# Kernel tuning notes

Measured on AMD Instinct MI355X. Metric: run time of the kernel, lower is better.

The kernel has to match this reference:

```python
import jax, jax.numpy as jnp
import numpy as np

HIDDEN = 1024
HEADS = 16
HEAD_DIM = HIDDEN // HEADS
GAMMA = 0.5
B, S = 2, 2048


def setup_inputs() -> dict:
    key = jax.random.key(0)
    ks = jax.random.split(key, 9)
    sc = 1.0 / np.sqrt(HIDDEN)
    x = jax.random.normal(ks[0], (B, S, HIDDEN), dtype=jnp.float32)
    attn_mask = jnp.zeros((S, S), dtype=bool)  # True = masked; all-False here
    Wq = jax.random.normal(ks[1], (HIDDEN, HIDDEN), dtype=jnp.float32) * sc
    bq = jnp.zeros((HIDDEN,), dtype=jnp.float32)
    Wk = jax.random.normal(ks[2], (HIDDEN, HIDDEN), dtype=jnp.float32) * sc
    bk = jnp.zeros((HIDDEN,), dtype=jnp.float32)
    Wv = jax.random.normal(ks[3], (HIDDEN, HIDDEN), dtype=jnp.float32) * sc
    bv = jnp.zeros((HIDDEN,), dtype=jnp.float32)
    Wo = jax.random.normal(ks[4], (HIDDEN, HIDDEN), dtype=jnp.float32) * sc
    bo = jnp.zeros((HIDDEN,), dtype=jnp.float32)
    return {"x": x, "attn_mask": attn_mask, "Wq": Wq, "bq": bq,
            "Wk": Wk, "bk": bk, "Wv": Wv, "bv": bv, "Wo": Wo, "bo": bo}


def reference(x, attn_mask, Wq, bq, Wk, bk, Wv, bv, Wo, bo):
    Bn, Sn, _ = x.shape
    # projections (torch Linear: x @ W.T + b), reshape to [B, H, S, Dh]
    def proj(W, b):
        y = x @ W.T + b
        return y.reshape(Bn, Sn, HEADS, HEAD_DIM).transpose(0, 2, 1, 3)
    q, k, v = proj(Wq, bq), proj(Wk, bk), proj(Wv, bv)
    scores = jnp.einsum('bhqd,bhkd->bhqk', q, k) / np.sqrt(HEAD_DIM)
    # diversity bias: cosine similarity of raw x (F.normalize eps=1e-12)
    normed = x / jnp.maximum(jnp.linalg.norm(x, axis=-1, keepdims=True), 1e-12)
    sim = jnp.einsum('bqd,bkd->bqk', normed, normed)
    scores = scores - GAMMA * sim[:, None, :, :]
    scores = jnp.where(attn_mask[None, None, :, :], -jnp.inf, scores)
    probs = jax.nn.softmax(scores, axis=-1)
    ctx = jnp.einsum('bhqk,bhkd->bhqd', probs, v)
    ctx = ctx.transpose(0, 2, 1, 3).reshape(Bn, Sn, HIDDEN)
    return ctx @ Wo.T + bo
```

## Files before the change

kernel.cpp:

```cpp
#include <hip/hip_runtime.h>

#define HID 1024
#define SEQ 2048
#define NB 2
#define NH 16
#define HD 64

#define C1 0.1803368801111204f
#define C2 0.7213475204444817f

typedef __attribute__((ext_vector_type(8))) short bf16x8;
typedef __attribute__((ext_vector_type(8))) unsigned short u16x8;
typedef __attribute__((ext_vector_type(4))) float f32x4;

__device__ __forceinline__ unsigned short f2bf(float f) {
  unsigned u = __builtin_bit_cast(unsigned, f);
  u += 0x7fffu + ((u >> 16) & 1u);
  return (unsigned short)(u >> 16);
}
__device__ __forceinline__ float bf2f(unsigned short u) {
  return __builtin_bit_cast(float, ((unsigned)u) << 16);
}

#define GLOAD16(gsrc, ldst)                                                     \
  __builtin_amdgcn_global_load_lds(                                             \
      (const __attribute__((address_space(1))) void*)(gsrc),                    \
      (__attribute__((address_space(3))) void*)(ldst), 16, 0, 0)

__global__ __launch_bounds__(256) void convert_w_kernel(
    const float* __restrict__ Wq, const float* __restrict__ Wk,
    const float* __restrict__ Wv, const float* __restrict__ Wo,
    unsigned short* __restrict__ Wb) {
  int i = blockIdx.x * 256 + threadIdx.x;
  const int per = (HID * HID) / 8;
  int m = i / per;
  const float* sp = (m == 0) ? Wq : (m == 1) ? Wk : (m == 2) ? Wv : Wo;
  int j = (i - m * per) * 8;
  const float4* p = reinterpret_cast<const float4*>(sp + j);
  float4 a = p[0], b = p[1];
  u16x8 o;
  o[0] = f2bf(a.x); o[1] = f2bf(a.y); o[2] = f2bf(a.z); o[3] = f2bf(a.w);
  o[4] = f2bf(b.x); o[5] = f2bf(b.y); o[6] = f2bf(b.z); o[7] = f2bf(b.w);
  *reinterpret_cast<u16x8*>(Wb + (size_t)i * 8) = o;
}

__global__ __launch_bounds__(256) void rownorm_kernel(
    const float* __restrict__ x, unsigned short* __restrict__ xb,
    unsigned short* __restrict__ nxb) {
  int row = blockIdx.x, tid = threadIdx.x;
  const float4 v = reinterpret_cast<const float4*>(x + (size_t)row * HID)[tid];
  float ss = v.x * v.x + v.y * v.y + v.z * v.z + v.w * v.w;
#pragma unroll
  for (int off = 32; off; off >>= 1) ss += __shfl_xor(ss, off, 64);
  __shared__ float wsum[4];
  if ((tid & 63) == 0) wsum[tid >> 6] = ss;
  __syncthreads();
  float tot = wsum[0] + wsum[1] + wsum[2] + wsum[3];
  float inv = 1.0f / fmaxf(sqrtf(tot), 1e-12f);
  ushort4 a, b;
  a.x = f2bf(v.x); a.y = f2bf(v.y); a.z = f2bf(v.z); a.w = f2bf(v.w);
  b.x = f2bf(v.x * inv); b.y = f2bf(v.y * inv);
  b.z = f2bf(v.z * inv); b.w = f2bf(v.w * inv);
  reinterpret_cast<ushort4*>(xb  + (size_t)row * HID)[tid] = a;
  reinterpret_cast<ushort4*>(nxb + (size_t)row * HID)[tid] = b;
}

template <int MODE>
__global__ __launch_bounds__(256) void gemm_nt(
    const unsigned short* __restrict__ A, long strideA,
    const unsigned short* __restrict__ B, long strideB,
    void* __restrict__ Cv, long strideC, int ldc,
    int M, int N, int K,
    const float* __restrict__ b0, const float* __restrict__ b1,
    const float* __restrict__ b2, const unsigned char* __restrict__ mask) {
  __shared__ __align__(16) unsigned short As[128][40];
  __shared__ __align__(16) unsigned short Bs[128][40];
  int tid = threadIdx.x, lane = tid & 63, wid = tid >> 6;
  int g = lane >> 4, lr = lane & 15;
  int wr = wid >> 1, wc = wid & 1;
  int m0 = blockIdx.y * 128, n0 = blockIdx.x * 128;
  const unsigned short* Ab = A + (size_t)blockIdx.z * strideA;
  const unsigned short* Bb = B + (size_t)blockIdx.z * strideB;
  f32x4 acc[4][4] = {};
  for (int k0 = 0; k0 < K; k0 += 32) {
#pragma unroll
    for (int p = 0; p < 2; p++) {
      int u = tid + p * 256;
      int row = u >> 2, chk = u & 3;
      *reinterpret_cast<u16x8*>(&As[row][chk * 8]) =
          *reinterpret_cast<const u16x8*>(Ab + (size_t)(m0 + row) * K + k0 + chk * 8);
      *reinterpret_cast<u16x8*>(&Bs[row][chk * 8]) =
          *reinterpret_cast<const u16x8*>(Bb + (size_t)(n0 + row) * K + k0 + chk * 8);
    }
    __syncthreads();
    bf16x8 af[4], bfr[4];
#pragma unroll
    for (int i = 0; i < 4; i++) {
      af[i]  = *reinterpret_cast<const bf16x8*>(&As[wr * 64 + i * 16 + lr][g * 8]);
      bfr[i] = *reinterpret_cast<const bf16x8*>(&Bs[wc * 64 + i * 16 + lr][g * 8]);
    }
#pragma unroll
    for (int i = 0; i < 4; i++)
#pragma unroll
      for (int j = 0; j < 4; j++)
        acc[i][j] = __builtin_amdgcn_mfma_f32_16x16x32_bf16(af[i], bfr[j], acc[i][j], 0, 0, 0);
    __syncthreads();
  }
#pragma unroll
  for (int i = 0; i < 4; i++)
#pragma unroll
    for (int j = 0; j < 4; j++) {
      int col = n0 + wc * 64 + j * 16 + lr;
#pragma unroll
      for (int r = 0; r < 4; r++) {
        int row = m0 + wr * 64 + i * 16 + 4 * g + r;
        float v = acc[i][j][r];
        if (MODE == 0) {
          const float* bp = (col < 1024) ? b0 : (col < 2048 ? b1 : b2);
          v += bp[col & 1023];
          ((unsigned short*)Cv)[(size_t)blockIdx.z * strideC + (size_t)row * ldc + col] = f2bf(v);
        } else if (MODE == 1) {
          float t = -C2 * v + (mask[(size_t)row * N + col] ? -1e30f : 0.0f);
          ((unsigned short*)Cv)[(size_t)blockIdx.z * strideC + (size_t)row * ldc + col] = f2bf(t);
        } else {
          v += b0[col];
          ((float*)Cv)[(size_t)blockIdx.z * strideC + (size_t)row * ldc + col] = v;
        }
      }
    }
}

__global__ __launch_bounds__(512) void flash_kernel(
    const unsigned short* __restrict__ QKV,
    const unsigned short* __restrict__ D2,
    unsigned short* __restrict__ ctxb) {
  int qt = blockIdx.x, h = blockIdx.y, b = blockIdx.z;
  int tid = threadIdx.x, wid = tid >> 6, lane = tid & 63;
  int g = lane >> 4, lr = lane & 15;
  __shared__ __align__(16) unsigned short Ks[2][64 * 64];
  __shared__ __align__(16) unsigned short Vt[2][64 * 64];
  __shared__ __align__(16) unsigned short Pl[8][16 * 72];
  const size_t ld = 3 * HID;
  const size_t bS = (size_t)b * SEQ;

  const unsigned short* qp = QKV + (bS + qt * 128 + wid * 16 + lr) * ld + h * HD;
  bf16x8 qf0 = *reinterpret_cast<const bf16x8*>(qp + g * 8);
  bf16x8 qf1 = *reinterpret_cast<const bf16x8*>(qp + 32 + g * 8);

  const unsigned short* gK = QKV + (bS + wid * 8 + (lane >> 3)) * ld + HID + h * HD
                             + (((lane & 7) ^ (lane >> 3)) << 3);
  const unsigned short* gV = QKV + (bS + (tid >> 3)) * ld + 2 * HID + h * HD + ((tid & 7) << 3);
  const int ch = tid & 7, kr3 = (tid >> 3) & 7, kb = tid >> 6;
  const int vtbase = ch * 512 + kr3;
  const int pre7 = (kb ^ ch) & 7;

  const unsigned short* bD = D2 + (size_t)b * SEQ * SEQ
                             + (size_t)(qt * 128 + wid * 16 + lr) * SEQ + 4 * g;

  GLOAD16(gK, &Ks[0][0] + wid * 512);
  {
    u16x8 vv = *reinterpret_cast<const u16x8*>(gV);
#pragma unroll
    for (int i = 0; i < 8; i++)
      Vt[0][vtbase + i * 64 + ((pre7 ^ i) << 3)] = vv[i];
  }
  __syncthreads();

  f32x4 acc[4] = {};
  float mrun = -1e30f, lrun = 0.0f;
  const int kb0 = lr * 64 + ((g ^ (lr & 7)) << 3);

  for (int kt = 0; kt < 32; ++kt) {
    const int cb = kt & 1;
    const unsigned short* ks = &Ks[cb][0];
    const unsigned short* vt = &Vt[cb][0];
    u16x8 vv2 = {};
    if (kt < 31) {
      GLOAD16(gK + (size_t)(kt + 1) * 64 * ld, &Ks[cb ^ 1][0] + wid * 512);
      vv2 = *reinterpret_cast<const u16x8*>(gV + (size_t)(kt + 1) * 64 * ld);
    }
    ushort4 bv4[4];
#pragma unroll
    for (int kc = 0; kc < 4; kc++)
      bv4[kc] = *reinterpret_cast<const ushort4*>(bD + kt * 64 + kc * 16);

    f32x4 s[4];
#pragma unroll
    for (int kc = 0; kc < 4; kc++) {
      bf16x8 kf0 = *reinterpret_cast<const bf16x8*>(ks + kc * 1024 + kb0);
      bf16x8 kf1 = *reinterpret_cast<const bf16x8*>(ks + kc * 1024 + (kb0 ^ 32));
      f32x4 z = {};
      z = __builtin_amdgcn_mfma_f32_16x16x32_bf16(kf0, qf0, z, 0, 0, 0);
      s[kc] = __builtin_amdgcn_mfma_f32_16x16x32_bf16(kf1, qf1, z, 0, 0, 0);
    }
    float mx = mrun;
#pragma unroll
    for (int kc = 0; kc < 4; kc++) {
      s[kc][0] = fmaf(s[kc][0], C1, bf2f(bv4[kc].x));
      s[kc][1] = fmaf(s[kc][1], C1, bf2f(bv4[kc].y));
      s[kc][2] = fmaf(s[kc][2], C1, bf2f(bv4[kc].z));
      s[kc][3] = fmaf(s[kc][3], C1, bf2f(bv4[kc].w));
      mx = fmaxf(mx, fmaxf(fmaxf(s[kc][0], s[kc][1]), fmaxf(s[kc][2], s[kc][3])));
    }
    mx = fmaxf(mx, __shfl_xor(mx, 16, 64));
    mx = fmaxf(mx, __shfl_xor(mx, 32, 64));
    float sc = exp2f(mrun - mx);
    mrun = mx;
    float rs = 0.0f;
#pragma unroll
    for (int kc = 0; kc < 4; kc++) {
      float p0 = exp2f(s[kc][0] - mx), p1 = exp2f(s[kc][1] - mx);
      float p2 = exp2f(s[kc][2] - mx), p3 = exp2f(s[kc][3] - mx);
      rs += (p0 + p1) + (p2 + p3);
      ushort4 pk;
      pk.x = f2bf(p0); pk.y = f2bf(p1); pk.z = f2bf(p2); pk.w = f2bf(p3);
      *reinterpret_cast<ushort4*>(&Pl[wid][lr * 72 + kc * 16 + 4 * g]) = pk;
    }
    rs += __shfl_xor(rs, 16, 64);
    rs += __shfl_xor(rs, 32, 64);
    lrun = lrun * sc + rs;
    float s0 = __shfl(sc, 4 * g + 0, 16), s1 = __shfl(sc, 4 * g + 1, 16);
    float s2 = __shfl(sc, 4 * g + 2, 16), s3 = __shfl(sc, 4 * g + 3, 16);
#pragma unroll
    for (int df = 0; df < 4; df++) {
      acc[df][0] *= s0; acc[df][1] *= s1; acc[df][2] *= s2; acc[df][3] *= s3;
    }
    if (kt < 31) {
#pragma unroll
      for (int i = 0; i < 8; i++)
        Vt[cb ^ 1][vtbase + i * 64 + ((pre7 ^ i) << 3)] = vv2[i];
    }
#pragma unroll
    for (int c2 = 0; c2 < 2; c2++) {
      bf16x8 pf = *reinterpret_cast<const bf16x8*>(&Pl[wid][lr * 72 + c2 * 32 + g * 8]);
#pragma unroll
      for (int df = 0; df < 4; df++) {
        int blk = ((4 * c2 + g) ^ (lr & 7) ^ ((df * 2 + (lr >> 3)) & 7)) & 7;
        bf16x8 vf = *reinterpret_cast<const bf16x8*>(vt + (df * 16 + lr) * 64 + (blk << 3));
        acc[df] = __builtin_amdgcn_mfma_f32_16x16x32_bf16(pf, vf, acc[df], 0, 0, 0);
      }
    }
    __syncthreads();
  }
  float l0 = 1.0f / __shfl(lrun, 4 * g + 0, 16);
  float l1 = 1.0f / __shfl(lrun, 4 * g + 1, 16);
  float l2 = 1.0f / __shfl(lrun, 4 * g + 2, 16);
  float l3 = 1.0f / __shfl(lrun, 4 * g + 3, 16);
  unsigned short* op = ctxb + (bS + qt * 128 + wid * 16 + 4 * g) * HID + h * HD + lr;
#pragma unroll
  for (int df = 0; df < 4; df++) {
    op[0 * HID + df * 16] = f2bf(acc[df][0] * l0);
    op[1 * HID + df * 16] = f2bf(acc[df][1] * l1);
    op[2 * HID + df * 16] = f2bf(acc[df][2] * l2);
    op[3 * HID + df * 16] = f2bf(acc[df][3] * l3);
  }
}

extern "C" void kernel_launch(void* const* d_in, const int* in_sizes, int n_in,
                              void* d_out, int out_size, void* d_ws, size_t ws_size,
                              hipStream_t stream) {
  const float* x = (const float*)d_in[0];
  const unsigned char* mask = (const unsigned char*)d_in[1];
  const float* Wq = (const float*)d_in[2];
  const float* bq = (const float*)d_in[3];
  const float* Wk = (const float*)d_in[4];
  const float* bk = (const float*)d_in[5];
  const float* Wv = (const float*)d_in[6];
  const float* bv = (const float*)d_in[7];
  const float* Wo = (const float*)d_in[8];
  const float* bo = (const float*)d_in[9];
  float* out = (float*)d_out;

  char* ws = (char*)d_ws;
  const size_t MiB = 1024 * 1024;
  unsigned short* xb  = (unsigned short*)(ws + 0 * MiB);
  unsigned short* nxb = (unsigned short*)(ws + 8 * MiB);
  unsigned short* Wb  = (unsigned short*)(ws + 16 * MiB);
  unsigned short* QKV = (unsigned short*)(ws + 24 * MiB);
  unsigned short* D2  = (unsigned short*)(ws + 48 * MiB);
  unsigned short* ctx = (unsigned short*)(ws + 64 * MiB);

  convert_w_kernel<<<2048, 256, 0, stream>>>(Wq, Wk, Wv, Wo, Wb);
  rownorm_kernel<<<NB * SEQ, 256, 0, stream>>>(x, xb, nxb);
  gemm_nt<0><<<dim3(24, 32, 1), 256, 0, stream>>>(
      xb, 0, Wb, 0, QKV, 0, 3 * HID, NB * SEQ, 3 * HID, HID, bq, bk, bv, nullptr);
  gemm_nt<1><<<dim3(16, 16, 2), 256, 0, stream>>>(
      nxb, (long)SEQ * HID, nxb, (long)SEQ * HID, D2, (long)SEQ * SEQ, SEQ,
      SEQ, SEQ, HID, nullptr, nullptr, nullptr, mask);
  flash_kernel<<<dim3(SEQ / 128, NH, NB), 512, 0, stream>>>(QKV, D2, ctx);
  gemm_nt<2><<<dim3(8, 32, 1), 256, 0, stream>>>(
      ctx, 0, Wb + (size_t)3 * HID * HID, 0, out, 0, HID, NB * SEQ, HID, HID,
      bo, nullptr, nullptr, nullptr);
}
```

Before: 231.4 us.

## Rework flash kernel with smaller blocks, lazy rescale, and MFMA row sums; GEMM direct-to-LDS loads

The flash attention kernel moves from 512-thread blocks covering 128 queries to 256-thread blocks covering 64 queries. It reorders the grid so heads vary fastest, which lets blocks sharing a query tile reuse the D2 bias in cache. It skips the online-softmax rescale unless the row max rises by more than a threshold, computes row sums with an MFMA against a ones vector, packs bf16 with a permute that truncates instead of rounding, and XOR-swizzles the P tile instead of padding it. The GEMM switches its tile loads to the direct global-to-LDS GLOAD16 macro with an unpadded layout, which may add LDS bank conflicts on the fragment reads. The lazy rescale and truncating bf16 conversion change numerics slightly.

```diff
diff --git a/kernel.cpp b/kernel.cpp
--- a/kernel.cpp
+++ b/kernel.cpp
@@ -73,31 +73,30 @@
     int M, int N, int K,
     const float* __restrict__ b0, const float* __restrict__ b1,
     const float* __restrict__ b2, const unsigned char* __restrict__ mask) {
-  __shared__ __align__(16) unsigned short As[128][40];
-  __shared__ __align__(16) unsigned short Bs[128][40];
+  __shared__ __align__(16) unsigned short As[128 * 32];
+  __shared__ __align__(16) unsigned short Bs[128 * 32];
   int tid = threadIdx.x, lane = tid & 63, wid = tid >> 6;
   int g = lane >> 4, lr = lane & 15;
   int wr = wid >> 1, wc = wid & 1;
   int m0 = blockIdx.y * 128, n0 = blockIdx.x * 128;
-  const unsigned short* Ab = A + (size_t)blockIdx.z * strideA;
-  const unsigned short* Bb = B + (size_t)blockIdx.z * strideB;
+  const unsigned short* Ab = A + (size_t)blockIdx.z * strideA
+      + (size_t)(m0 + wid * 32 + (lane >> 2)) * K + (lane & 3) * 8;
+  const unsigned short* Bb = B + (size_t)blockIdx.z * strideB
+      + (size_t)(n0 + wid * 32 + (lane >> 2)) * K + (lane & 3) * 8;
+  unsigned short* la = As + wid * 1024;
+  unsigned short* lb = Bs + wid * 1024;
   f32x4 acc[4][4] = {};
   for (int k0 = 0; k0 < K; k0 += 32) {
-#pragma unroll
-    for (int p = 0; p < 2; p++) {
-      int u = tid + p * 256;
-      int row = u >> 2, chk = u & 3;
-      *reinterpret_cast<u16x8*>(&As[row][chk * 8]) =
-          *reinterpret_cast<const u16x8*>(Ab + (size_t)(m0 + row) * K + k0 + chk * 8);
-      *reinterpret_cast<u16x8*>(&Bs[row][chk * 8]) =
-          *reinterpret_cast<const u16x8*>(Bb + (size_t)(n0 + row) * K + k0 + chk * 8);
-    }
+    GLOAD16(Ab + k0, la);
+    GLOAD16(Ab + 16 * K + k0, la + 512);
+    GLOAD16(Bb + k0, lb);
+    GLOAD16(Bb + 16 * K + k0, lb + 512);
     __syncthreads();
     bf16x8 af[4], bfr[4];
 #pragma unroll
     for (int i = 0; i < 4; i++) {
-      af[i]  = *reinterpret_cast<const bf16x8*>(&As[wr * 64 + i * 16 + lr][g * 8]);
-      bfr[i] = *reinterpret_cast<const bf16x8*>(&Bs[wc * 64 + i * 16 + lr][g * 8]);
+      af[i]  = *reinterpret_cast<const bf16x8*>(&As[(wr * 64 + i * 16 + lr) * 32 + g * 8]);
+      bfr[i] = *reinterpret_cast<const bf16x8*>(&Bs[(wc * 64 + i * 16 + lr) * 32 + g * 8]);
     }
 #pragma unroll
     for (int i = 0; i < 4; i++)
@@ -130,59 +129,77 @@
     }
 }
 
-__global__ __launch_bounds__(512) void flash_kernel(
+__global__ __launch_bounds__(256, 4) void flash_kernel(
     const unsigned short* __restrict__ QKV,
     const unsigned short* __restrict__ D2,
     unsigned short* __restrict__ ctxb) {
-  int qt = blockIdx.x, h = blockIdx.y, b = blockIdx.z;
+  int h = blockIdx.x, qt = blockIdx.y, b = blockIdx.z;
   int tid = threadIdx.x, wid = tid >> 6, lane = tid & 63;
   int g = lane >> 4, lr = lane & 15;
   __shared__ __align__(16) unsigned short Ks[2][64 * 64];
   __shared__ __align__(16) unsigned short Vt[2][64 * 64];
-  __shared__ __align__(16) unsigned short Pl[8][16 * 72];
+  __shared__ __align__(16) unsigned short Pl[4][16 * 64];
   const size_t ld = 3 * HID;
   const size_t bS = (size_t)b * SEQ;
-
-  const unsigned short* qp = QKV + (bS + qt * 128 + wid * 16 + lr) * ld + h * HD;
-  bf16x8 qf0 = *reinterpret_cast<const bf16x8*>(qp + g * 8);
-  bf16x8 qf1 = *reinterpret_cast<const bf16x8*>(qp + 32 + g * 8);
-
-  const unsigned short* gK = QKV + (bS + wid * 8 + (lane >> 3)) * ld + HID + h * HD
-                             + (((lane & 7) ^ (lane >> 3)) << 3);
-  const unsigned short* gV = QKV + (bS + (tid >> 3)) * ld + 2 * HID + h * HD + ((tid & 7) << 3);
-  const int ch = tid & 7, kr3 = (tid >> 3) & 7, kb = tid >> 6;
+  const int qbase = qt * 64 + wid * 16;
+
+  const unsigned short* qp = QKV + (bS + qbase + lr) * ld + h * HD + g * 8;
+  bf16x8 qf0 = *reinterpret_cast<const bf16x8*>(qp);
+  bf16x8 qf1 = *reinterpret_cast<const bf16x8*>(qp + 32);
+
+  const unsigned short* gK0 = QKV + (bS + wid * 16 + (lane >> 3)) * ld + HID + h * HD
+                              + (((lane & 7) ^ (lane >> 3)) << 3);
+  const unsigned short* gK1 = gK0 + 8 * ld;
+
+  const int vr0 = tid >> 3, ch = tid & 7;
+  const unsigned short* gV0 = QKV + (bS + vr0) * ld + 2 * HID + h * HD + (ch << 3);
+  const unsigned short* gV1 = gV0 + 32 * ld;
+  const int kr3 = vr0 & 7;
+  const int kb0v = vr0 >> 3, kb1v = kb0v + 4;
   const int vtbase = ch * 512 + kr3;
-  const int pre7 = (kb ^ ch) & 7;
+  const int pre0 = (kb0v ^ ch) & 7, pre1 = (kb1v ^ ch) & 7;
 
   const unsigned short* bD = D2 + (size_t)b * SEQ * SEQ
-                             + (size_t)(qt * 128 + wid * 16 + lr) * SEQ + 4 * g;
-
-  GLOAD16(gK, &Ks[0][0] + wid * 512);
+                             + (size_t)(qbase + lr) * SEQ + 4 * g;
+
+  GLOAD16(gK0, &Ks[0][wid * 1024]);
+  GLOAD16(gK1, &Ks[0][wid * 1024 + 512]);
   {
-    u16x8 vv = *reinterpret_cast<const u16x8*>(gV);
-#pragma unroll
-    for (int i = 0; i < 8; i++)
-      Vt[0][vtbase + i * 64 + ((pre7 ^ i) << 3)] = vv[i];
+    u16x8 v0 = *reinterpret_cast<const u16x8*>(gV0);
+    u16x8 v1 = *reinterpret_cast<const u16x8*>(gV1);
+#pragma unroll
+    for (int i = 0; i < 8; i++) {
+      Vt[0][vtbase + i * 64 + ((pre0 ^ i) << 3)] = v0[i];
+      Vt[0][vtbase + i * 64 + ((pre1 ^ i) << 3)] = v1[i];
+    }
   }
   __syncthreads();
 
   f32x4 acc[4] = {};
-  float mrun = -1e30f, lrun = 0.0f;
+  f32x4 rsacc = {};
+  float mrun = -1e30f;
   const int kb0 = lr * 64 + ((g ^ (lr & 7)) << 3);
+  const int plw = lr * 64;
+  const int plm = (lr & 7) << 3;
+  bf16x8 ones;
+#pragma unroll
+  for (int i = 0; i < 8; i++) ones[i] = 0x3F80;
 
   for (int kt = 0; kt < 32; ++kt) {
     const int cb = kt & 1;
     const unsigned short* ks = &Ks[cb][0];
     const unsigned short* vt = &Vt[cb][0];
-    u16x8 vv2 = {};
+    u16x8 vv0 = {}, vv1 = {};
     if (kt < 31) {
-      GLOAD16(gK + (size_t)(kt + 1) * 64 * ld, &Ks[cb ^ 1][0] + wid * 512);
-      vv2 = *reinterpret_cast<const u16x8*>(gV + (size_t)(kt + 1) * 64 * ld);
-    }
-    ushort4 bv4[4];
+      GLOAD16(gK0 + (size_t)(kt + 1) * 64 * ld, &Ks[cb ^ 1][wid * 1024]);
+      GLOAD16(gK1 + (size_t)(kt + 1) * 64 * ld, &Ks[cb ^ 1][wid * 1024 + 512]);
+      vv0 = *reinterpret_cast<const u16x8*>(gV0 + (size_t)(kt + 1) * 64 * ld);
+      vv1 = *reinterpret_cast<const u16x8*>(gV1 + (size_t)(kt + 1) * 64 * ld);
+    }
+    ushort4 bv[4];
 #pragma unroll
     for (int kc = 0; kc < 4; kc++)
-      bv4[kc] = *reinterpret_cast<const ushort4*>(bD + kt * 64 + kc * 16);
+      bv[kc] = *reinterpret_cast<const ushort4*>(bD + kt * 64 + kc * 16);
 
     f32x4 s[4];
 #pragma unroll
@@ -193,46 +210,63 @@
       z = __builtin_amdgcn_mfma_f32_16x16x32_bf16(kf0, qf0, z, 0, 0, 0);
       s[kc] = __builtin_amdgcn_mfma_f32_16x16x32_bf16(kf1, qf1, z, 0, 0, 0);
     }
-    float mx = mrun;
+    float mx;
+    {
+      float m01, m23;
+#pragma unroll
+      for (int kc = 0; kc < 4; kc++) {
+        s[kc][0] = fmaf(s[kc][0], C1, bf2f(bv[kc].x));
+        s[kc][1] = fmaf(s[kc][1], C1, bf2f(bv[kc].y));
+        s[kc][2] = fmaf(s[kc][2], C1, bf2f(bv[kc].z));
+        s[kc][3] = fmaf(s[kc][3], C1, bf2f(bv[kc].w));
+      }
+      m01 = fmaxf(fmaxf(s[0][0], s[0][1]), fmaxf(s[0][2], s[0][3]));
+      m23 = fmaxf(fmaxf(s[1][0], s[1][1]), fmaxf(s[1][2], s[1][3]));
+      m01 = fmaxf(m01, fmaxf(fmaxf(s[2][0], s[2][1]), fmaxf(s[2][2], s[2][3])));
+      m23 = fmaxf(m23, fmaxf(fmaxf(s[3][0], s[3][1]), fmaxf(s[3][2], s[3][3])));
+      mx = fmaxf(m01, m23);
+    }
+    if (!__all(mx <= mrun + 8.0f)) {
+      float M = mx;
+      M = fmaxf(M, __shfl_xor(M, 16, 64));
+      M = fmaxf(M, __shfl_xor(M, 32, 64));
+      M = fmaxf(M, mrun);
+      float sc = exp2f(mrun - M);
+      mrun = M;
+      float s0 = __shfl(sc, 4 * g + 0, 16), s1 = __shfl(sc, 4 * g + 1, 16);
+      float s2 = __shfl(sc, 4 * g + 2, 16), s3 = __shfl(sc, 4 * g + 3, 16);
+#pragma unroll
+      for (int df = 0; df < 4; df++) {
+        acc[df][0] *= s0; acc[df][1] *= s1;
+        acc[df][2] *= s2; acc[df][3] *= s3;
+      }
+      rsacc[0] *= s0; rsacc[1] *= s1; rsacc[2] *= s2; rsacc[3] *= s3;
+    }
 #pragma unroll
     for (int kc = 0; kc < 4; kc++) {
-      s[kc][0] = fmaf(s[kc][0], C1, bf2f(bv4[kc].x));
-      s[kc][1] = fmaf(s[kc][1], C1, bf2f(bv4[kc].y));
-      s[kc][2] = fmaf(s[kc][2], C1, bf2f(bv4[kc].z));
-      s[kc][3] = fmaf(s[kc][3], C1, bf2f(bv4[kc].w));
-      mx = fmaxf(mx, fmaxf(fmaxf(s[kc][0], s[kc][1]), fmaxf(s[kc][2], s[kc][3])));
-    }
-    mx = fmaxf(mx, __shfl_xor(mx, 16, 64));
-    mx = fmaxf(mx, __shfl_xor(mx, 32, 64));
-    float sc = exp2f(mrun - mx);
-    mrun = mx;
-    float rs = 0.0f;
-#pragma unroll
-    for (int kc = 0; kc < 4; kc++) {
-      float p0 = exp2f(s[kc][0] - mx), p1 = exp2f(s[kc][1] - mx);
-      float p2 = exp2f(s[kc][2] - mx), p3 = exp2f(s[kc][3] - mx);
-      rs += (p0 + p1) + (p2 + p3);
-      ushort4 pk;
-      pk.x = f2bf(p0); pk.y = f2bf(p1); pk.z = f2bf(p2); pk.w = f2bf(p3);
-      *reinterpret_cast<ushort4*>(&Pl[wid][lr * 72 + kc * 16 + 4 * g]) = pk;
-    }
-    rs += __shfl_xor(rs, 16, 64);
-    rs += __shfl_xor(rs, 32, 64);
-    lrun = lrun * sc + rs;
-    float s0 = __shfl(sc, 4 * g + 0, 16), s1 = __shfl(sc, 4 * g + 1, 16);
-    float s2 = __shfl(sc, 4 * g + 2, 16), s3 = __shfl(sc, 4 * g + 3, 16);
-#pragma unroll
-    for (int df = 0; df < 4; df++) {
-      acc[df][0] *= s0; acc[df][1] *= s1; acc[df][2] *= s2; acc[df][3] *= s3;
+      float p0 = exp2f(s[kc][0] - mrun);
+      float p1 = exp2f(s[kc][1] - mrun);
+      float p2 = exp2f(s[kc][2] - mrun);
+      float p3 = exp2f(s[kc][3] - mrun);
+      uint2 w;
+      w.x = __builtin_amdgcn_perm(__builtin_bit_cast(unsigned, p1),
+                                  __builtin_bit_cast(unsigned, p0), 0x07060302u);
+      w.y = __builtin_amdgcn_perm(__builtin_bit_cast(unsigned, p3),
+                                  __builtin_bit_cast(unsigned, p2), 0x07060302u);
+      *reinterpret_cast<uint2*>(&Pl[wid][plw + ((kc * 16 + 4 * g) ^ plm)]) = w;
     }
     if (kt < 31) {
 #pragma unroll
-      for (int i = 0; i < 8; i++)
-        Vt[cb ^ 1][vtbase + i * 64 + ((pre7 ^ i) << 3)] = vv2[i];
+      for (int i = 0; i < 8; i++) {
+        Vt[cb ^ 1][vtbase + i * 64 + ((pre0 ^ i) << 3)] = vv0[i];
+        Vt[cb ^ 1][vtbase + i * 64 + ((pre1 ^ i) << 3)] = vv1[i];
+      }
     }
 #pragma unroll
     for (int c2 = 0; c2 < 2; c2++) {
-      bf16x8 pf = *reinterpret_cast<const bf16x8*>(&Pl[wid][lr * 72 + c2 * 32 + g * 8]);
+      bf16x8 pf = *reinterpret_cast<const bf16x8*>(
+          &Pl[wid][plw + ((c2 * 32 + g * 8) ^ plm)]);
+      rsacc = __builtin_amdgcn_mfma_f32_16x16x32_bf16(pf, ones, rsacc, 0, 0, 0);
 #pragma unroll
       for (int df = 0; df < 4; df++) {
         int blk = ((4 * c2 + g) ^ (lr & 7) ^ ((df * 2 + (lr >> 3)) & 7)) & 7;
@@ -242,11 +276,9 @@
     }
     __syncthreads();
   }
-  float l0 = 1.0f / __shfl(lrun, 4 * g + 0, 16);
-  float l1 = 1.0f / __shfl(lrun, 4 * g + 1, 16);
-  float l2 = 1.0f / __shfl(lrun, 4 * g + 2, 16);
-  float l3 = 1.0f / __shfl(lrun, 4 * g + 3, 16);
-  unsigned short* op = ctxb + (bS + qt * 128 + wid * 16 + 4 * g) * HID + h * HD + lr;
+  float l0 = 1.0f / rsacc[0], l1 = 1.0f / rsacc[1];
+  float l2 = 1.0f / rsacc[2], l3 = 1.0f / rsacc[3];
+  unsigned short* op = ctxb + (bS + qbase + 4 * g) * HID + h * HD + lr;
 #pragma unroll
   for (int df = 0; df < 4; df++) {
     op[0 * HID + df * 16] = f2bf(acc[df][0] * l0);
@@ -287,7 +319,7 @@
   gemm_nt<1><<<dim3(16, 16, 2), 256, 0, stream>>>(
       nxb, (long)SEQ * HID, nxb, (long)SEQ * HID, D2, (long)SEQ * SEQ, SEQ,
       SEQ, SEQ, HID, nullptr, nullptr, nullptr, mask);
-  flash_kernel<<<dim3(SEQ / 128, NH, NB), 512, 0, stream>>>(QKV, D2, ctx);
+  flash_kernel<<<dim3(NH, SEQ / 64, NB), 256, 0, stream>>>(QKV, D2, ctx);
   gemm_nt<2><<<dim3(8, 32, 1), 256, 0, stream>>>(
       ctx, 0, Wb + (size_t)3 * HID * HID, 0, out, 0, HID, NB * SEQ, HID, HID,
       bo, nullptr, nullptr, nullptr);
```

Result: faster. 211.9 us (-8.4%).
